# Kernel optimization log

Measured on AMD Instinct MI355X. Metric: run time of the kernel, lower is better.

The kernel has to match this reference:

```python
import jax, jax.numpy as jnp
import numpy as np

B, N, L, E = 4, 8, 2048, 16384
CH = [128, 256, 256, 256]
EPS = 1e-5
USE_MAX = True


def setup_inputs() -> dict:
    key = jax.random.key(0)
    ks = jax.random.split(key, 10)
    d = {}
    d["x"] = jax.random.normal(ks[0], (B, N, CH[0], L), jnp.float32)
    d["edge_index"] = jax.random.randint(ks[1], (2, E), 0, L, dtype=jnp.int32)
    wspecs = [("W1", CH[0], CH[1]), ("W2", CH[1], CH[2]), ("W3", CH[2], CH[3]),
              ("W1s", CH[0], CH[1]), ("W2s", CH[1], CH[2]), ("W3s", CH[2], CH[3])]
    for i, (nm, ci, co) in enumerate(wspecs):
        std = (2.0 / (ci + co)) ** 0.5  # xavier_normal
        d[nm] = std * jax.random.normal(ks[2 + i], (ci, co), jnp.float32)
        d["b" + nm[1:]] = jnp.zeros((co,), jnp.float32)
    for nm, co in [("1", CH[1]), ("2", CH[2]), ("3", CH[3]),
                   ("1s", CH[1]), ("2s", CH[2]), ("3s", CH[3])]:
        d["g" + nm] = jnp.ones((co,), jnp.float32)
        d["be" + nm] = jnp.zeros((co,), jnp.float32)
    return d


def _gcn_norm(edge_index, num_nodes):
    # PyG gcn_norm with improved=True: A_hat = A + 2I, sym normalization.
    src, dst = edge_index[0], edge_index[1]
    loop = jnp.arange(num_nodes, dtype=src.dtype)
    src = jnp.concatenate([src, loop])
    dst = jnp.concatenate([dst, loop])
    w = jnp.concatenate([jnp.ones((edge_index.shape[1],), jnp.float32),
                         jnp.full((num_nodes,), 2.0, jnp.float32)])
    deg = jnp.zeros((num_nodes,), jnp.float32).at[dst].add(w)
    dis = jnp.where(deg > 0, jax.lax.rsqrt(deg), 0.0)
    return src, dst, dis[src] * w * dis[dst]


def _gcn(h, W, bias, src, dst, norm, num_nodes):
    # h: [G, L, Cin] node features for G independent copies of the shared graph
    hw = h @ W  # [G, L, Cout]
    msgs = hw[:, src, :] * norm[None, :, None]  # gather along nodes
    agg = jnp.zeros((h.shape[0], num_nodes, W.shape[1]), h.dtype).at[:, dst].add(msgs)
    return agg + bias


def _bn(x, g, be):
    # x: [Nb, C, L]; training-mode BatchNorm1d over (Nb, L) per channel
    m = x.mean(axis=(0, 2), keepdims=True)
    v = x.var(axis=(0, 2), keepdims=True)
    return g[None, :, None] * (x - m) * jax.lax.rsqrt(v + EPS) + be[None, :, None]


def _forward(x, edge_index, params):
    b, n, c, l = x.shape
    src, dst, norm = _gcn_norm(edge_index, l)
    xo = None
    for (W, bias, Ws, bs, g, be, gs, bes) in params:
        # per-element branch
        h = x.reshape(b * n, x.shape[2], l).transpose(0, 2, 1)  # [b*n, L, C]
        x1 = _gcn(h, W, bias, src, dst, norm, l).transpose(0, 2, 1)  # [b*n, Cout, L]
        x1 = _bn(x1, g, be)
        # symmetric pooled branch
        xp = jnp.max(x, axis=1) if USE_MAX else jnp.sum(x, axis=1)  # [b, C, L]
        x2 = _gcn(xp.transpose(0, 2, 1), Ws, bs, src, dst, norm, l).transpose(0, 2, 1)
        x2 = _bn(x2, gs, bes)
        co = x2.shape[1]
        x2 = jnp.broadcast_to(x2[:, None], (b, n, co, l)).reshape(b * n, co, l)
        xo = jax.nn.relu(x1 + x2)  # [b*n, Cout, L]
        x = xo.reshape(b, n, co, l)
    return xo  # final output is [b*n, CH[3], L] (not reshaped back)


def reference(x, edge_index, W1, b1, W2, b2, W3, b3, W1s, b1s, W2s, b2s, W3s, b3s,
              g1, be1, g2, be2, g3, be3, g1s, be1s, g2s, be2s, g3s, be3s):
    params = [(W1, b1, W1s, b1s, g1, be1, g1s, be1s),
              (W2, b2, W2s, b2s, g2, be2, g2s, be2s),
              (W3, b3, W3s, b3s, g3, be3, g3s, be3s)]
    return _forward(x, edge_index, params)
```

## Files before the change

kernel.cpp:

```cpp
#include <hip/hip_runtime.h>
#include <math.h>

#define LNODES 2048
#define NEDGE 16384
#define GBIG 32
#define GSM 4
#define NCOUT 256
#define BN_EPS 1e-5f
#define ND 32

typedef unsigned short u16;
typedef __attribute__((ext_vector_type(8))) short bf16x8;
typedef __attribute__((ext_vector_type(4))) float f32x4;

__device__ __forceinline__ unsigned pk2(float a, float b) {
  unsigned ua = __float_as_uint(a); ua += 0x7fffu + ((ua >> 16) & 1u);
  unsigned ub = __float_as_uint(b); ub += 0x7fffu + ((ub >> 16) & 1u);
  return (ua >> 16) | (ub & 0xffff0000u);
}
__device__ __forceinline__ float blo(unsigned u) { return __uint_as_float(u << 16); }
__device__ __forceinline__ float bhi(unsigned u) { return __uint_as_float(u & 0xffff0000u); }


__global__ __launch_bounds__(256) void count_deg_k(const int* __restrict__ ei,
                                                   float* __restrict__ deg,
                                                   int* __restrict__ cnt) {
  int e = blockIdx.x * 256 + threadIdx.x;
  if (e < NEDGE) {
    int d = ei[NEDGE + e];
    atomicAdd(&deg[d], 1.0f);
    atomicAdd(&cnt[d], 1);
  }
}

__global__ __launch_bounds__(256) void dis_k(const float* __restrict__ deg,
                                             float* __restrict__ dis,
                                             float* __restrict__ selfn) {
  int i = blockIdx.x * 256 + threadIdx.x;
  if (i < LNODES) {
    float di = rsqrtf(deg[i] + 2.0f);
    dis[i] = di;
    selfn[i] = 2.0f * di * di;
  }
}

__global__ __launch_bounds__(256) void scan_k(const int* __restrict__ cnt,
                                              int* __restrict__ rp) {
  __shared__ int part[256];
  int t = threadIdx.x;
  int base = t * 8;
  int loc[8];
  int s = 0;
#pragma unroll
  for (int j = 0; j < 8; ++j) { loc[j] = s; s += cnt[base + j]; }
  part[t] = s;
  __syncthreads();
  for (int off = 1; off < 256; off <<= 1) {
    int v = (t >= off) ? part[t - off] : 0;
    __syncthreads();
    part[t] += v;
    __syncthreads();
  }
  int excl = (t == 0) ? 0 : part[t - 1];
#pragma unroll
  for (int j = 0; j < 8; ++j) rp[base + j] = excl + loc[j];
  if (t == 255) rp[LNODES] = part[255];
}

__global__ __launch_bounds__(256) void fill_k(const int* __restrict__ ei,
                                              const int* __restrict__ rp,
                                              int* __restrict__ fillc,
                                              const float* __restrict__ dis,
                                              int* __restrict__ col,
                                              float* __restrict__ wn) {
  int e = blockIdx.x * 256 + threadIdx.x;
  if (e < NEDGE) {
    int s = ei[e], d = ei[NEDGE + e];
    int pos = rp[d] + atomicAdd(&fillc[d], 1);
    col[pos] = s;
    wn[pos] = dis[s] * dis[d];
  }
}

__global__ __launch_bounds__(256) void trans_k(const float* __restrict__ X,
                                               u16* __restrict__ XT, int Cin) {
  __shared__ float T[64][65];
  const int g = blockIdx.z;
  const int n0 = blockIdx.x * 64;
  const int c0 = blockIdx.y * 64;
  const int tr = threadIdx.x >> 4;
  const int tc = (threadIdx.x & 15) * 4;
#pragma unroll
  for (int p = 0; p < 4; ++p) {
    int ci = c0 + tr + p * 16;
    float4 v = *reinterpret_cast<const float4*>(&X[((size_t)g * Cin + ci) * LNODES + n0 + tc]);
    T[tr + p * 16][tc + 0] = v.x; T[tr + p * 16][tc + 1] = v.y;
    T[tr + p * 16][tc + 2] = v.z; T[tr + p * 16][tc + 3] = v.w;
  }
  __syncthreads();
#pragma unroll
  for (int p = 0; p < 4; ++p) {
    int nd = tr + p * 16;
    uint2 o = {pk2(T[tc + 0][nd], T[tc + 1][nd]), pk2(T[tc + 2][nd], T[tc + 3][nd])};
    *reinterpret_cast<uint2*>(&XT[((size_t)g * LNODES + n0 + nd) * Cin + c0 + tc]) = o;
  }
}

struct WCvt {
  const float* src[6];
  u16* dst[6];
  int ci[6];
};
__global__ __launch_bounds__(256) void cvtw_all_k(WCvt wp) {
  __shared__ float T[64][65];
  const int w = blockIdx.z;
  const int Ci = wp.ci[w];
  const int ci0 = blockIdx.y * 64;
  if (ci0 >= Ci) return;
  const float* W = wp.src[w];
  u16* WT = wp.dst[w];
  const int co0 = blockIdx.x * 64;
  const int tr = threadIdx.x >> 4;
  const int tc = (threadIdx.x & 15) * 4;
#pragma unroll
  for (int p = 0; p < 4; ++p) {
    int ci = ci0 + tr + p * 16;
    float4 v = *reinterpret_cast<const float4*>(&W[(size_t)ci * NCOUT + co0 + tc]);
    T[tr + p * 16][tc + 0] = v.x; T[tr + p * 16][tc + 1] = v.y;
    T[tr + p * 16][tc + 2] = v.z; T[tr + p * 16][tc + 3] = v.w;
  }
  __syncthreads();
#pragma unroll
  for (int p = 0; p < 4; ++p) {
    int co = tr + p * 16;
    uint2 o = {pk2(T[tc + 0][co], T[tc + 1][co]), pk2(T[tc + 2][co], T[tc + 3][co])};
    *reinterpret_cast<uint2*>(&WT[(size_t)(co0 + co) * Ci + ci0 + tc]) = o;
  }
}

__global__ __launch_bounds__(256) void pool_bf_k(const u16* __restrict__ X,
                                                 u16* __restrict__ XP, int per) {
  int i = blockIdx.x * 256 + threadIdx.x;
  size_t f = (size_t)i * 8;
  int b = (int)(f / per);
  size_t rem = f - (size_t)b * per;
  const u16* base = X + (size_t)b * 8 * per + rem;
  uint4 u = *reinterpret_cast<const uint4*>(base);
  float m0 = blo(u.x), m1 = bhi(u.x), m2 = blo(u.y), m3 = bhi(u.y);
  float m4 = blo(u.z), m5 = bhi(u.z), m6 = blo(u.w), m7 = bhi(u.w);
#pragma unroll
  for (int j = 1; j < 8; ++j) {
    uint4 v = *reinterpret_cast<const uint4*>(base + (size_t)j * per);
    m0 = fmaxf(m0, blo(v.x)); m1 = fmaxf(m1, bhi(v.x));
    m2 = fmaxf(m2, blo(v.y)); m3 = fmaxf(m3, bhi(v.y));
    m4 = fmaxf(m4, blo(v.z)); m5 = fmaxf(m5, bhi(v.z));
    m6 = fmaxf(m6, blo(v.w)); m7 = fmaxf(m7, bhi(v.w));
  }
  uint4 o = {pk2(m0, m1), pk2(m2, m3), pk2(m4, m5), pk2(m6, m7)};
  *reinterpret_cast<uint4*>(XP + (size_t)b * per + rem) = o;
}

__device__ __forceinline__ void coef_ld(const float* __restrict__ st,
                                        const float* __restrict__ ga,
                                        const float* __restrict__ be,
                                        const float* __restrict__ gs,
                                        const float* __restrict__ bes,
                                        float* lk1, float* lk2, float* lcc, int t) {
  float sA = 0.f, qA = 0.f, sB = 0.f, qB = 0.f;
#pragma unroll
  for (int x = 0; x < 8; ++x) {
    sA += st[x * NCOUT + t];
    qA += st[2048 + x * NCOUT + t];
    sB += st[4096 + x * NCOUT + t];
    qB += st[6144 + x * NCOUT + t];
  }
  const float c1 = (float)(GBIG * LNODES), c2 = (float)(GSM * LNODES);
  float mA = sA / c1;
  float vA = qA / c1 - mA * mA;
  float kA = ga[t] * rsqrtf(vA + BN_EPS);
  float mB = sB / c2;
  float vB = qB / c2 - mB * mB;
  float kB = gs[t] * rsqrtf(vB + BN_EPS);
  lk1[t] = kA;
  lk2[t] = kB;
  lcc[t] = be[t] - kA * mA + bes[t] - kB * mB;
}

template <int MODE>
__global__ __launch_bounds__(256) void gemm2_k(const u16* __restrict__ B1,
                                               const u16* __restrict__ B2,
                                               const float* __restrict__ st,
                                               const float* __restrict__ ga,
                                               const float* __restrict__ be,
                                               const float* __restrict__ gs,
                                               const float* __restrict__ bes,
                                               const u16* __restrict__ WbT,
                                               const u16* __restrict__ WsT,
                                               u16* __restrict__ HW1,
                                               u16* __restrict__ hw2) {
  constexpr int Cin = (MODE == 0) ? 128 : 256;
  constexpr int BT = 64 * Cin;
  constexpr int EPI = 64 * 264;
  constexpr int SMSZ = (BT > EPI) ? BT : EPI;
  __shared__ u16 smem[SMSZ];
  __shared__ float lk1[NCOUT], lk2[NCOUT], lcc[NCOUT];
  const int z = blockIdx.z;
  const bool sym = z < GSM;
  const int g = sym ? z : z - GSM;
  const u16* Wmat = sym ? WsT : WbT;
  u16* out = sym ? hw2 : HW1;
  const int n0 = blockIdx.x * 64;
  const int t = threadIdx.x;
  constexpr int OPR = Cin / 8;
  constexpr int RPI = 256 / OPR;
  constexpr int NIT = 64 / RPI;
  const int ro = t / OPR;
  const int ch8 = (t % OPR) * 8;

  float K1[8], K2[8], CC[8];
  if constexpr (MODE == 1) {
    coef_ld(st, ga, be, gs, bes, lk1, lk2, lcc, t);
    __syncthreads();
#pragma unroll
    for (int j = 0; j < 8; ++j) { K1[j] = lk1[ch8 + j]; K2[j] = lk2[ch8 + j]; CC[j] = lcc[ch8 + j]; }
  }

#define BIDX(r, c) ((((r) * Cin) + (c)) ^ (((r) & 7) << 3))

  if constexpr (MODE == 0) {
    const u16* src = (sym ? B2 : B1) + (size_t)g * LNODES * Cin;
#pragma unroll
    for (int it = 0; it < NIT; ++it) {
      int row = it * RPI + ro;
      uint4 v = *reinterpret_cast<const uint4*>(&src[(size_t)(n0 + row) * Cin + ch8]);
      *reinterpret_cast<uint4*>(&smem[BIDX(row, ch8)]) = v;
    }
  } else if (!sym) {
    const size_t b1o = ((size_t)g * LNODES + n0) * NCOUT + ch8;
    const size_t b2o = ((size_t)(g >> 3) * LNODES + n0) * NCOUT + ch8;
#pragma unroll
    for (int it = 0; it < NIT; ++it) {
      int row = it * RPI + ro;
      uint4 a1 = *reinterpret_cast<const uint4*>(&B1[b1o + (size_t)row * NCOUT]);
      uint4 a2 = *reinterpret_cast<const uint4*>(&B2[b2o + (size_t)row * NCOUT]);
      float o0 = fmaxf(K1[0] * blo(a1.x) + K2[0] * blo(a2.x) + CC[0], 0.f);
      float o1 = fmaxf(K1[1] * bhi(a1.x) + K2[1] * bhi(a2.x) + CC[1], 0.f);
      float o2 = fmaxf(K1[2] * blo(a1.y) + K2[2] * blo(a2.y) + CC[2], 0.f);
      float o3 = fmaxf(K1[3] * bhi(a1.y) + K2[3] * bhi(a2.y) + CC[3], 0.f);
      float o4 = fmaxf(K1[4] * blo(a1.z) + K2[4] * blo(a2.z) + CC[4], 0.f);
      float o5 = fmaxf(K1[5] * bhi(a1.z) + K2[5] * bhi(a2.z) + CC[5], 0.f);
      float o6 = fmaxf(K1[6] * blo(a1.w) + K2[6] * blo(a2.w) + CC[6], 0.f);
      float o7 = fmaxf(K1[7] * bhi(a1.w) + K2[7] * bhi(a2.w) + CC[7], 0.f);
      uint4 ov = {pk2(o0, o1), pk2(o2, o3), pk2(o4, o5), pk2(o6, o7)};
      *reinterpret_cast<uint4*>(&smem[BIDX(row, ch8)]) = ov;
    }
  } else {
    const size_t b2o = ((size_t)g * LNODES + n0) * NCOUT + ch8;
    const size_t a1b = ((size_t)(g * 8) * LNODES + n0) * NCOUT + ch8;
    const size_t nstep = (size_t)LNODES * NCOUT;
    for (int it = 0; it < NIT; ++it) {
      int row = it * RPI + ro;
      uint4 a2 = *reinterpret_cast<const uint4*>(&B2[b2o + (size_t)row * NCOUT]);
      float t0 = K2[0] * blo(a2.x) + CC[0], t1 = K2[1] * bhi(a2.x) + CC[1];
      float t2 = K2[2] * blo(a2.y) + CC[2], t3 = K2[3] * bhi(a2.y) + CC[3];
      float t4 = K2[4] * blo(a2.z) + CC[4], t5 = K2[5] * bhi(a2.z) + CC[5];
      float t6 = K2[6] * blo(a2.w) + CC[6], t7 = K2[7] * bhi(a2.w) + CC[7];
      float m0 = 0.f, m1 = 0.f, m2 = 0.f, m3 = 0.f, m4 = 0.f, m5 = 0.f, m6 = 0.f, m7 = 0.f;
#pragma unroll
      for (int n = 0; n < 8; ++n) {
        uint4 a1 = *reinterpret_cast<const uint4*>(&B1[a1b + n * nstep + (size_t)row * NCOUT]);
        m0 = fmaxf(m0, K1[0] * blo(a1.x) + t0); m1 = fmaxf(m1, K1[1] * bhi(a1.x) + t1);
        m2 = fmaxf(m2, K1[2] * blo(a1.y) + t2); m3 = fmaxf(m3, K1[3] * bhi(a1.y) + t3);
        m4 = fmaxf(m4, K1[4] * blo(a1.z) + t4); m5 = fmaxf(m5, K1[5] * bhi(a1.z) + t5);
        m6 = fmaxf(m6, K1[6] * blo(a1.w) + t6); m7 = fmaxf(m7, K1[7] * bhi(a1.w) + t7);
      }
      uint4 ov = {pk2(m0, m1), pk2(m2, m3), pk2(m4, m5), pk2(m6, m7)};
      *reinterpret_cast<uint4*>(&smem[BIDX(row, ch8)]) = ov;
    }
  }
  __syncthreads();

  const int wv = t >> 6;
  const int lane = t & 63;
  const int q = lane >> 4, l = lane & 15;
  f32x4 zero = {0.f, 0.f, 0.f, 0.f};
  f32x4 acc[4][4];
#pragma unroll
  for (int i = 0; i < 4; ++i)
#pragma unroll
    for (int j = 0; j < 4; ++j) acc[i][j] = zero;

  const u16* Wfrag = Wmat + (size_t)(wv * 64 + l) * Cin + q * 8;
#pragma unroll
  for (int k0 = 0; k0 < Cin; k0 += 32) {
    bf16x8 af[4], bx[4];
#pragma unroll
    for (int fi = 0; fi < 4; ++fi)
      af[fi] = *reinterpret_cast<const bf16x8*>(&Wfrag[(size_t)(fi * 16) * Cin + k0]);
#pragma unroll
    for (int fj = 0; fj < 4; ++fj) {
      int brow = fj * 16 + l;
      bx[fj] = *reinterpret_cast<const bf16x8*>(&smem[(brow * Cin + k0 + q * 8) ^ ((brow & 7) << 3)]);
    }
#pragma unroll
    for (int fi = 0; fi < 4; ++fi)
#pragma unroll
      for (int fj = 0; fj < 4; ++fj)
        acc[fi][fj] = __builtin_amdgcn_mfma_f32_16x16x32_bf16(af[fi], bx[fj], acc[fi][fj], 0, 0, 0);
  }
#undef BIDX

  __syncthreads();
  u16* Csh = smem;
#pragma unroll
  for (int fi = 0; fi < 4; ++fi) {
#pragma unroll
    for (int fj = 0; fj < 4; ++fj) {
      int co_l = wv * 64 + fi * 16 + q * 4;
      int nd_l = fj * 16 + l;
      uint2 pkd = {pk2(acc[fi][fj][0], acc[fi][fj][1]),
                   pk2(acc[fi][fj][2], acc[fi][fj][3])};
      *reinterpret_cast<uint2*>(&Csh[nd_l * 264 + co_l]) = pkd;
    }
  }
  __syncthreads();
#pragma unroll
  for (int p = 0; p < 8; ++p) {
    int idx = p * 256 + t;
    int nd = idx >> 5;
    int c8 = (idx & 31) * 8;
    uint4 v = *reinterpret_cast<const uint4*>(&Csh[nd * 264 + c8]);
    *reinterpret_cast<uint4*>(&out[((size_t)g * LNODES + n0 + nd) * NCOUT + c8]) = v;
  }
}

__global__ __launch_bounds__(256) void agg_comb_k(const u16* __restrict__ HW1,
                                                  const u16* __restrict__ hw2,
                                                  const int* __restrict__ col,
                                                  const float* __restrict__ wn,
                                                  const int* __restrict__ rp,
                                                  const float* __restrict__ selfn,
                                                  u16* __restrict__ AGG1,
                                                  u16* __restrict__ agg2,
                                                  float* __restrict__ st) {
  __shared__ float lsum[8][NCOUT], lsq[8][NCOUT];
  const int bid = blockIdx.x;
  const int t = threadIdx.x;
  const int wv = t >> 6;
  float* sumO;
  float* sqO;
  int shard;
  if (bid < 1024) {
    int slot = bid >> 3;
    int chunk = slot & 63;
    int g0 = (bid & 7) + 8 * (slot >> 6);
    const int d0 = chunk * ND;
    const int h = (t >> 5) & 1;
    const int ch = (t & 31) * 8;
    const u16* baseh = HW1 + (size_t)(g0 + 16 * h) * LNODES * NCOUT;
    u16* outh = AGG1 + (size_t)(g0 + 16 * h) * LNODES * NCOUT;
    float s0 = 0.f, s1 = 0.f, s2 = 0.f, s3 = 0.f, s4 = 0.f, s5 = 0.f, s6 = 0.f, s7 = 0.f;
    float q0 = 0.f, q1 = 0.f, q2 = 0.f, q3 = 0.f, q4 = 0.f, q5 = 0.f, q6 = 0.f, q7 = 0.f;
    for (int i = wv; i < ND; i += 4) {
      int d = d0 + i;
      int e0 = rp[d], e1 = rp[d + 1];
      float sw = selfn[d];
      uint4 u = *reinterpret_cast<const uint4*>(&baseh[(size_t)d * NCOUT + ch]);
      float a0 = sw * blo(u.x), a1 = sw * bhi(u.x), a2 = sw * blo(u.y), a3 = sw * bhi(u.y);
      float a4 = sw * blo(u.z), a5 = sw * bhi(u.z), a6 = sw * blo(u.w), a7 = sw * bhi(u.w);
      int e = e0;
      const int e4 = e0 + ((e1 - e0) & ~3);
      for (; e < e4; e += 4) {
        int i0 = col[e + 0], i1 = col[e + 1], i2 = col[e + 2], i3 = col[e + 3];
        float w0 = wn[e + 0], w1 = wn[e + 1], w2 = wn[e + 2], w3 = wn[e + 3];
        uint4 v0 = *reinterpret_cast<const uint4*>(&baseh[(size_t)i0 * NCOUT + ch]);
        uint4 v1 = *reinterpret_cast<const uint4*>(&baseh[(size_t)i1 * NCOUT + ch]);
        uint4 v2 = *reinterpret_cast<const uint4*>(&baseh[(size_t)i2 * NCOUT + ch]);
        uint4 v3 = *reinterpret_cast<const uint4*>(&baseh[(size_t)i3 * NCOUT + ch]);
        a0 += w0 * blo(v0.x); a1 += w0 * bhi(v0.x); a2 += w0 * blo(v0.y); a3 += w0 * bhi(v0.y);
        a4 += w0 * blo(v0.z); a5 += w0 * bhi(v0.z); a6 += w0 * blo(v0.w); a7 += w0 * bhi(v0.w);
        a0 += w1 * blo(v1.x); a1 += w1 * bhi(v1.x); a2 += w1 * blo(v1.y); a3 += w1 * bhi(v1.y);
        a4 += w1 * blo(v1.z); a5 += w1 * bhi(v1.z); a6 += w1 * blo(v1.w); a7 += w1 * bhi(v1.w);
        a0 += w2 * blo(v2.x); a1 += w2 * bhi(v2.x); a2 += w2 * blo(v2.y); a3 += w2 * bhi(v2.y);
        a4 += w2 * blo(v2.z); a5 += w2 * bhi(v2.z); a6 += w2 * blo(v2.w); a7 += w2 * bhi(v2.w);
        a0 += w3 * blo(v3.x); a1 += w3 * bhi(v3.x); a2 += w3 * blo(v3.y); a3 += w3 * bhi(v3.y);
        a4 += w3 * blo(v3.z); a5 += w3 * bhi(v3.z); a6 += w3 * blo(v3.w); a7 += w3 * bhi(v3.w);
      }
      for (; e < e1; ++e) {
        int ci = col[e];
        float w = wn[e];
        uint4 v = *reinterpret_cast<const uint4*>(&baseh[(size_t)ci * NCOUT + ch]);
        a0 += w * blo(v.x); a1 += w * bhi(v.x); a2 += w * blo(v.y); a3 += w * bhi(v.y);
        a4 += w * blo(v.z); a5 += w * bhi(v.z); a6 += w * blo(v.w); a7 += w * bhi(v.w);
      }
      uint4 o = {pk2(a0, a1), pk2(a2, a3), pk2(a4, a5), pk2(a6, a7)};
      *reinterpret_cast<uint4*>(&outh[(size_t)d * NCOUT + ch]) = o;
      s0 += a0; s1 += a1; s2 += a2; s3 += a3; s4 += a4; s5 += a5; s6 += a6; s7 += a7;
      q0 += a0 * a0; q1 += a1 * a1; q2 += a2 * a2; q3 += a3 * a3;
      q4 += a4 * a4; q5 += a5 * a5; q6 += a6 * a6; q7 += a7 * a7;
    }
    int row = wv * 2 + h;
    float4 sa = {s0, s1, s2, s3}, sb = {s4, s5, s6, s7};
    float4 qa = {q0, q1, q2, q3}, qb = {q4, q5, q6, q7};
    *reinterpret_cast<float4*>(&lsum[row][ch]) = sa;
    *reinterpret_cast<float4*>(&lsum[row][ch + 4]) = sb;
    *reinterpret_cast<float4*>(&lsq[row][ch]) = qa;
    *reinterpret_cast<float4*>(&lsq[row][ch + 4]) = qb;
    sumO = st; sqO = st + 2048; shard = (bid & 7) * NCOUT;
  } else {
    int b2 = bid - 1024;
    int g = b2 & (GSM - 1);
    int chunk = b2 >> 2;
    const int d0 = chunk * ND;
    const int lc = (t & 63) * 4;
    const u16* base = hw2 + (size_t)g * LNODES * NCOUT;
    float4 s = {0.f, 0.f, 0.f, 0.f}, qq = {0.f, 0.f, 0.f, 0.f};
    for (int i = wv; i < ND; i += 4) {
      int d = d0 + i;
      int e0 = rp[d], e1 = rp[d + 1];
      float sw = selfn[d];
      uint2 u = *reinterpret_cast<const uint2*>(&base[(size_t)d * NCOUT + lc]);
      float4 a = {sw * blo(u.x), sw * bhi(u.x), sw * blo(u.y), sw * bhi(u.y)};
      int e = e0;
      const int e4 = e0 + ((e1 - e0) & ~3);
      for (; e < e4; e += 4) {
        int i0 = col[e + 0], i1 = col[e + 1], i2 = col[e + 2], i3 = col[e + 3];
        float w0 = wn[e + 0], w1 = wn[e + 1], w2 = wn[e + 2], w3 = wn[e + 3];
        uint2 v0 = *reinterpret_cast<const uint2*>(&base[(size_t)i0 * NCOUT + lc]);
        uint2 v1 = *reinterpret_cast<const uint2*>(&base[(size_t)i1 * NCOUT + lc]);
        uint2 v2 = *reinterpret_cast<const uint2*>(&base[(size_t)i2 * NCOUT + lc]);
        uint2 v3 = *reinterpret_cast<const uint2*>(&base[(size_t)i3 * NCOUT + lc]);
        a.x += w0 * blo(v0.x); a.y += w0 * bhi(v0.x); a.z += w0 * blo(v0.y); a.w += w0 * bhi(v0.y);
        a.x += w1 * blo(v1.x); a.y += w1 * bhi(v1.x); a.z += w1 * blo(v1.y); a.w += w1 * bhi(v1.y);
        a.x += w2 * blo(v2.x); a.y += w2 * bhi(v2.x); a.z += w2 * blo(v2.y); a.w += w2 * bhi(v2.y);
        a.x += w3 * blo(v3.x); a.y += w3 * bhi(v3.x); a.z += w3 * blo(v3.y); a.w += w3 * bhi(v3.y);
      }
      for (; e < e1; ++e) {
        float w = wn[e];
        uint2 v = *reinterpret_cast<const uint2*>(&base[(size_t)col[e] * NCOUT + lc]);
        a.x += w * blo(v.x); a.y += w * bhi(v.x); a.z += w * blo(v.y); a.w += w * bhi(v.y);
      }
      uint2 o = {pk2(a.x, a.y), pk2(a.z, a.w)};
      *reinterpret_cast<uint2*>(&agg2[((size_t)g * LNODES + d) * NCOUT + lc]) = o;
      s.x += a.x; s.y += a.y; s.z += a.z; s.w += a.w;
      qq.x += a.x * a.x; qq.y += a.y * a.y; qq.z += a.z * a.z; qq.w += a.w * a.w;
    }
    *reinterpret_cast<float4*>(&lsum[wv][lc]) = s;
    *reinterpret_cast<float4*>(&lsq[wv][lc]) = qq;
    float4 z4 = {0.f, 0.f, 0.f, 0.f};
    *reinterpret_cast<float4*>(&lsum[wv + 4][lc]) = z4;
    *reinterpret_cast<float4*>(&lsq[wv + 4][lc]) = z4;
    sumO = st + 4096; sqO = st + 6144; shard = (b2 & 7) * NCOUT;
  }
  __syncthreads();
  float ts = 0.f, tq = 0.f;
#pragma unroll
  for (int r = 0; r < 8; ++r) {
    ts += lsum[r][t];
    tq += lsq[r][t];
  }
  atomicAdd(&sumO[shard + t], ts);
  atomicAdd(&sqO[shard + t], tq);
}

__global__ __launch_bounds__(256) void fuse_tr_bf_k(const u16* __restrict__ A1,
                                                    const u16* __restrict__ A2,
                                                    const float* __restrict__ st,
                                                    const float* __restrict__ ga,
                                                    const float* __restrict__ be,
                                                    const float* __restrict__ gs,
                                                    const float* __restrict__ bes,
                                                    float* __restrict__ O) {
  __shared__ float T[64][65];
  __shared__ float lk1[NCOUT], lk2[NCOUT], lcc[NCOUT];
  const int g = blockIdx.z;
  const int d0 = blockIdx.x * 64;
  const int c0 = blockIdx.y * 64;
  const int b = g >> 3;
  const int t = threadIdx.x;
  coef_ld(st, ga, be, gs, bes, lk1, lk2, lcc, t);
  __syncthreads();
  const int tr = t >> 4;
  const int tc = (t & 15) * 4;
#pragma unroll
  for (int p = 0; p < 4; ++p) {
    int d = d0 + tr + p * 16;
    uint2 a1 = *reinterpret_cast<const uint2*>(&A1[((size_t)g * LNODES + d) * NCOUT + c0 + tc]);
    uint2 a2 = *reinterpret_cast<const uint2*>(&A2[((size_t)b * LNODES + d) * NCOUT + c0 + tc]);
    int cb = c0 + tc;
    T[tr + p * 16][tc + 0] = fmaxf(lk1[cb+0] * blo(a1.x) + lk2[cb+0] * blo(a2.x) + lcc[cb+0], 0.f);
    T[tr + p * 16][tc + 1] = fmaxf(lk1[cb+1] * bhi(a1.x) + lk2[cb+1] * bhi(a2.x) + lcc[cb+1], 0.f);
    T[tr + p * 16][tc + 2] = fmaxf(lk1[cb+2] * blo(a1.y) + lk2[cb+2] * blo(a2.y) + lcc[cb+2], 0.f);
    T[tr + p * 16][tc + 3] = fmaxf(lk1[cb+3] * bhi(a1.y) + lk2[cb+3] * bhi(a2.y) + lcc[cb+3], 0.f);
  }
  __syncthreads();
#pragma unroll
  for (int p = 0; p < 4; ++p) {
    int c = tr + p * 16;
    float4 o = {T[tc + 0][c], T[tc + 1][c], T[tc + 2][c], T[tc + 3][c]};
    *reinterpret_cast<float4*>(&O[((size_t)g * NCOUT + c0 + c) * LNODES + d0 + tc]) = o;
  }
}


extern "C" void kernel_launch(void* const* d_in, const int* in_sizes, int n_in,
                              void* d_out, int out_size, void* d_ws, size_t ws_size,
                              hipStream_t stream) {
  const float* x_in = (const float*)d_in[0];
  const int* ei = (const int*)d_in[1];
  const float* W[3]   = {(const float*)d_in[2],  (const float*)d_in[4],  (const float*)d_in[6]};
  const float* Wsym[3]= {(const float*)d_in[8],  (const float*)d_in[10], (const float*)d_in[12]};
  const float* ga[3]  = {(const float*)d_in[14], (const float*)d_in[16], (const float*)d_in[18]};
  const float* be[3]  = {(const float*)d_in[15], (const float*)d_in[17], (const float*)d_in[19]};
  const float* gs[3]  = {(const float*)d_in[20], (const float*)d_in[22], (const float*)d_in[24]};
  const float* bes[3] = {(const float*)d_in[21], (const float*)d_in[23], (const float*)d_in[25]};

  const size_t EBIG = (size_t)GBIG * LNODES * NCOUT;
  const size_t ESM = (size_t)GSM * LNODES * NCOUT;
  char* p = (char*)d_ws;
  u16* XT0  = (u16*)p; p += (size_t)GBIG * LNODES * 128 * 2;
  u16* AGG1 = (u16*)p; p += EBIG * 2;
  u16* agg2 = (u16*)p; p += ESM * 2;
  u16* xp   = (u16*)p; p += ESM * 2;
  u16* hw2  = (u16*)p; p += ESM * 2;
  u16* WbT[3], *WsT[3];
  for (int i = 0; i < 3; ++i) { WbT[i] = (u16*)p; p += NCOUT * NCOUT * 2; }
  for (int i = 0; i < 3; ++i) { WsT[i] = (u16*)p; p += NCOUT * NCOUT * 2; }
  int*   rp   = (int*)p;   p += 2064 * 4;
  float* dis  = (float*)p; p += LNODES * 4;
  float* selfn= (float*)p; p += LNODES * 4;
  char* zbase = p;
  float* deg  = (float*)p; p += LNODES * 4;
  int*   cnt  = (int*)p;   p += LNODES * 4;
  int*   fillc= (int*)p;   p += LNODES * 4;
  int*   col  = (int*)p;   p += (NEDGE + 8) * 4;
  float* wn   = (float*)p; p += (NEDGE + 8) * 4;
  float* stats= (float*)p; p += 3 * 4 * 2048 * 4;
  size_t zsize = (size_t)(p - zbase);

  u16* HW1 = (u16*)d_out;
  float* stL[3] = {stats, stats + 8192, stats + 16384};

  hipMemsetAsync(zbase, 0, zsize, stream);
  count_deg_k<<<NEDGE / 256, 256, 0, stream>>>(ei, deg, cnt);
  dis_k<<<LNODES / 256, 256, 0, stream>>>(deg, dis, selfn);
  scan_k<<<1, 256, 0, stream>>>(cnt, rp);
  fill_k<<<NEDGE / 256, 256, 0, stream>>>(ei, rp, fillc, dis, col, wn);
  WCvt wc;
  for (int i = 0; i < 3; ++i) {
    wc.src[i] = W[i];     wc.dst[i] = WbT[i];     wc.ci[i] = (i == 0) ? 128 : 256;
    wc.src[3 + i] = Wsym[i]; wc.dst[3 + i] = WsT[i]; wc.ci[3 + i] = (i == 0) ? 128 : 256;
  }
  cvtw_all_k<<<dim3(4, 4, 6), 256, 0, stream>>>(wc);
  trans_k<<<dim3(LNODES / 64, 128 / 64, GBIG), 256, 0, stream>>>(x_in, XT0, 128);
  pool_bf_k<<<GSM * 128 * LNODES / 8 / 256, 256, 0, stream>>>(XT0, xp, 128 * LNODES);

  dim3 ggrid(LNODES / 64, 1, GBIG + GSM);
  gemm2_k<0><<<ggrid, 256, 0, stream>>>(XT0, xp, nullptr, nullptr, nullptr, nullptr,
                                        nullptr, WbT[0], WsT[0], HW1, hw2);
  agg_comb_k<<<1280, 256, 0, stream>>>(HW1, hw2, col, wn, rp, selfn, AGG1, agg2, stL[0]);
  gemm2_k<1><<<ggrid, 256, 0, stream>>>(AGG1, agg2, stL[0], ga[0], be[0], gs[0], bes[0],
                                        WbT[1], WsT[1], HW1, hw2);
  agg_comb_k<<<1280, 256, 0, stream>>>(HW1, hw2, col, wn, rp, selfn, AGG1, agg2, stL[1]);
  gemm2_k<1><<<ggrid, 256, 0, stream>>>(AGG1, agg2, stL[1], ga[1], be[1], gs[1], bes[1],
                                        WbT[2], WsT[2], HW1, hw2);
  agg_comb_k<<<1280, 256, 0, stream>>>(HW1, hw2, col, wn, rp, selfn, AGG1, agg2, stL[2]);
  fuse_tr_bf_k<<<dim3(LNODES / 64, NCOUT / 64, GBIG), 256, 0, stream>>>(
      AGG1, agg2, stL[2], ga[2], be[2], gs[2], bes[2], (float*)d_out);
}
```

Before: 357.7 us.

## Stage weight K-tiles into LDS via direct global-to-LDS loads in GEMM

Weights are pre-converted into a K-tiled, XOR-swizzled layout with 32-wide K slices. The GEMM stages each 256x32 slice into shared memory with global_load_lds, then reads A fragments from LDS instead of issuing strided global loads per wave. The goal is to cut uncoalesced global weight traffic and latency in the MFMA loop. The cost is two barriers per K step and 16 KB of extra LDS per block, which may lower occupancy and serialise loading with compute.

```diff
diff --git a/kernel.cpp b/kernel.cpp
--- a/kernel.cpp
+++ b/kernel.cpp
@@ -20,6 +20,12 @@
 }
 __device__ __forceinline__ float blo(unsigned u) { return __uint_as_float(u << 16); }
 __device__ __forceinline__ float bhi(unsigned u) { return __uint_as_float(u & 0xffff0000u); }
+
+__device__ __forceinline__ void gl16(const u16* g, u16* l) {
+  __builtin_amdgcn_global_load_lds(
+      (const __attribute__((address_space(1))) void*)g,
+      (__attribute__((address_space(3))) void*)l, 16, 0, 0);
+}
 
 
 __global__ __launch_bounds__(256) void count_deg_k(const int* __restrict__ ei,
@@ -130,11 +136,16 @@
     T[tr + p * 16][tc + 2] = v.z; T[tr + p * 16][tc + 3] = v.w;
   }
   __syncthreads();
+  const int ci = ci0 + tc;
+  const int kt = ci >> 5;
+  const int kk = ci & 31;
 #pragma unroll
   for (int p = 0; p < 4; ++p) {
-    int co = tr + p * 16;
-    uint2 o = {pk2(T[tc + 0][co], T[tc + 1][co]), pk2(T[tc + 2][co], T[tc + 3][co])};
-    *reinterpret_cast<uint2*>(&WT[(size_t)(co0 + co) * Ci + ci0 + tc]) = o;
+    int co = co0 + tr + p * 16;
+    uint2 o = {pk2(T[tc + 0][co - co0], T[tc + 1][co - co0]),
+               pk2(T[tc + 2][co - co0], T[tc + 3][co - co0])};
+    size_t idx = (size_t)kt * 8192 + (unsigned)((co * 32 + kk) ^ ((co & 7) << 3));
+    *reinterpret_cast<uint2*>(&WT[idx]) = o;
   }
 }
 
@@ -187,7 +198,7 @@
 }
 
 template <int MODE>
-__global__ __launch_bounds__(256) void gemm2_k(const u16* __restrict__ B1,
+__global__ __launch_bounds__(256) void gemm3_k(const u16* __restrict__ B1,
                                                const u16* __restrict__ B2,
                                                const float* __restrict__ st,
                                                const float* __restrict__ ga,
@@ -199,15 +210,15 @@
                                                u16* __restrict__ HW1,
                                                u16* __restrict__ hw2) {
   constexpr int Cin = (MODE == 0) ? 128 : 256;
-  constexpr int BT = 64 * Cin;
+  constexpr int BSH = 64 * Cin;
   constexpr int EPI = 64 * 264;
-  constexpr int SMSZ = (BT > EPI) ? BT : EPI;
-  __shared__ u16 smem[SMSZ];
+  constexpr int BASE = (BSH > EPI) ? BSH : EPI;
+  __shared__ __align__(16) u16 smem[BASE + 8192];
   __shared__ float lk1[NCOUT], lk2[NCOUT], lcc[NCOUT];
+  u16* Wsh = smem + BASE;
   const int z = blockIdx.z;
   const bool sym = z < GSM;
   const int g = sym ? z : z - GSM;
-  const u16* Wmat = sym ? WsT : WbT;
   u16* out = sym ? hw2 : HW1;
   const int n0 = blockIdx.x * 64;
   const int t = threadIdx.x;
@@ -227,15 +238,40 @@
 
 #define BIDX(r, c) ((((r) * Cin) + (c)) ^ (((r) & 7) << 3))
 
-  if constexpr (MODE == 0) {
-    const u16* src = (sym ? B2 : B1) + (size_t)g * LNODES * Cin;
-#pragma unroll
-    for (int it = 0; it < NIT; ++it) {
-      int row = it * RPI + ro;
-      uint4 v = *reinterpret_cast<const uint4*>(&src[(size_t)(n0 + row) * Cin + ch8]);
-      *reinterpret_cast<uint4*>(&smem[BIDX(row, ch8)]) = v;
-    }
-  } else if (!sym) {
+  if (MODE == 0 || sym) {
+    if constexpr (MODE == 0) {
+      const u16* src = (sym ? B2 : B1) + ((size_t)g * LNODES + n0) * Cin + ch8;
+#pragma unroll
+      for (int it = 0; it < NIT; ++it) {
+        int row = it * RPI + ro;
+        uint4 v = *reinterpret_cast<const uint4*>(&src[(size_t)row * Cin]);
+        *reinterpret_cast<uint4*>(&smem[BIDX(row, ch8)]) = v;
+      }
+    } else {
+      const size_t b2o = ((size_t)g * LNODES + n0) * NCOUT + ch8;
+      const size_t a1b = ((size_t)(g * 8) * LNODES + n0) * NCOUT + ch8;
+      const size_t nstep = (size_t)LNODES * NCOUT;
+      for (int it = 0; it < NIT; ++it) {
+        int row = it * RPI + ro;
+        uint4 a2 = *reinterpret_cast<const uint4*>(&B2[b2o + (size_t)row * NCOUT]);
+        float t0 = K2[0] * blo(a2.x) + CC[0], t1 = K2[1] * bhi(a2.x) + CC[1];
+        float t2 = K2[2] * blo(a2.y) + CC[2], t3 = K2[3] * bhi(a2.y) + CC[3];
+        float t4 = K2[4] * blo(a2.z) + CC[4], t5 = K2[5] * bhi(a2.z) + CC[5];
+        float t6 = K2[6] * blo(a2.w) + CC[6], t7 = K2[7] * bhi(a2.w) + CC[7];
+        float m0 = 0.f, m1 = 0.f, m2 = 0.f, m3 = 0.f, m4 = 0.f, m5 = 0.f, m6 = 0.f, m7 = 0.f;
+#pragma unroll
+        for (int n = 0; n < 8; ++n) {
+          uint4 a1 = *reinterpret_cast<const uint4*>(&B1[a1b + n * nstep + (size_t)row * NCOUT]);
+          m0 = fmaxf(m0, K1[0] * blo(a1.x) + t0); m1 = fmaxf(m1, K1[1] * bhi(a1.x) + t1);
+          m2 = fmaxf(m2, K1[2] * blo(a1.y) + t2); m3 = fmaxf(m3, K1[3] * bhi(a1.y) + t3);
+          m4 = fmaxf(m4, K1[4] * blo(a1.z) + t4); m5 = fmaxf(m5, K1[5] * bhi(a1.z) + t5);
+          m6 = fmaxf(m6, K1[6] * blo(a1.w) + t6); m7 = fmaxf(m7, K1[7] * bhi(a1.w) + t7);
+        }
+        uint4 ov = {pk2(m0, m1), pk2(m2, m3), pk2(m4, m5), pk2(m6, m7)};
+        *reinterpret_cast<uint4*>(&smem[BIDX(row, ch8)]) = ov;
+      }
+    }
+  } else {
     const size_t b1o = ((size_t)g * LNODES + n0) * NCOUT + ch8;
     const size_t b2o = ((size_t)(g >> 3) * LNODES + n0) * NCOUT + ch8;
 #pragma unroll
@@ -254,31 +290,7 @@
       uint4 ov = {pk2(o0, o1), pk2(o2, o3), pk2(o4, o5), pk2(o6, o7)};
       *reinterpret_cast<uint4*>(&smem[BIDX(row, ch8)]) = ov;
     }
-  } else {
-    const size_t b2o = ((size_t)g * LNODES + n0) * NCOUT + ch8;
-    const size_t a1b = ((size_t)(g * 8) * LNODES + n0) * NCOUT + ch8;
-    const size_t nstep = (size_t)LNODES * NCOUT;
-    for (int it = 0; it < NIT; ++it) {
-      int row = it * RPI + ro;
-      uint4 a2 = *reinterpret_cast<const uint4*>(&B2[b2o + (size_t)row * NCOUT]);
-      float t0 = K2[0] * blo(a2.x) + CC[0], t1 = K2[1] * bhi(a2.x) + CC[1];
-      float t2 = K2[2] * blo(a2.y) + CC[2], t3 = K2[3] * bhi(a2.y) + CC[3];
-      float t4 = K2[4] * blo(a2.z) + CC[4], t5 = K2[5] * bhi(a2.z) + CC[5];
-      float t6 = K2[6] * blo(a2.w) + CC[6], t7 = K2[7] * bhi(a2.w) + CC[7];
-      float m0 = 0.f, m1 = 0.f, m2 = 0.f, m3 = 0.f, m4 = 0.f, m5 = 0.f, m6 = 0.f, m7 = 0.f;
-#pragma unroll
-      for (int n = 0; n < 8; ++n) {
-        uint4 a1 = *reinterpret_cast<const uint4*>(&B1[a1b + n * nstep + (size_t)row * NCOUT]);
-        m0 = fmaxf(m0, K1[0] * blo(a1.x) + t0); m1 = fmaxf(m1, K1[1] * bhi(a1.x) + t1);
-        m2 = fmaxf(m2, K1[2] * blo(a1.y) + t2); m3 = fmaxf(m3, K1[3] * bhi(a1.y) + t3);
-        m4 = fmaxf(m4, K1[4] * blo(a1.z) + t4); m5 = fmaxf(m5, K1[5] * bhi(a1.z) + t5);
-        m6 = fmaxf(m6, K1[6] * blo(a1.w) + t6); m7 = fmaxf(m7, K1[7] * bhi(a1.w) + t7);
-      }
-      uint4 ov = {pk2(m0, m1), pk2(m2, m3), pk2(m4, m5), pk2(m6, m7)};
-      *reinterpret_cast<uint4*>(&smem[BIDX(row, ch8)]) = ov;
-    }
-  }
-  __syncthreads();
+  }
 
   const int wv = t >> 6;
   const int lane = t & 63;
@@ -290,17 +302,25 @@
 #pragma unroll
     for (int j = 0; j < 4; ++j) acc[i][j] = zero;
 
-  const u16* Wfrag = Wmat + (size_t)(wv * 64 + l) * Cin + q * 8;
-#pragma unroll
-  for (int k0 = 0; k0 < Cin; k0 += 32) {
+  const u16* Wmat = sym ? WsT : WbT;
+#pragma unroll
+  for (int kt = 0; kt < Cin / 32; ++kt) {
+    __syncthreads();
+    const u16* ws = Wmat + (size_t)kt * 8192;
+#pragma unroll
+    for (int c = 0; c < 4; ++c)
+      gl16(ws + c * 2048 + t * 8, &Wsh[c * 2048 + t * 8]);
+    __syncthreads();
     bf16x8 af[4], bx[4];
 #pragma unroll
-    for (int fi = 0; fi < 4; ++fi)
-      af[fi] = *reinterpret_cast<const bf16x8*>(&Wfrag[(size_t)(fi * 16) * Cin + k0]);
+    for (int fi = 0; fi < 4; ++fi) {
+      int row = wv * 64 + fi * 16 + l;
+      af[fi] = *reinterpret_cast<const bf16x8*>(&Wsh[(row * 32 + q * 8) ^ ((row & 7) << 3)]);
+    }
 #pragma unroll
     for (int fj = 0; fj < 4; ++fj) {
       int brow = fj * 16 + l;
-      bx[fj] = *reinterpret_cast<const bf16x8*>(&smem[(brow * Cin + k0 + q * 8) ^ ((brow & 7) << 3)]);
+      bx[fj] = *reinterpret_cast<const bf16x8*>(&smem[BIDX(brow, kt * 32 + q * 8)]);
     }
 #pragma unroll
     for (int fi = 0; fi < 4; ++fi)
@@ -556,13 +576,13 @@
   pool_bf_k<<<GSM * 128 * LNODES / 8 / 256, 256, 0, stream>>>(XT0, xp, 128 * LNODES);
 
   dim3 ggrid(LNODES / 64, 1, GBIG + GSM);
-  gemm2_k<0><<<ggrid, 256, 0, stream>>>(XT0, xp, nullptr, nullptr, nullptr, nullptr,
+  gemm3_k<0><<<ggrid, 256, 0, stream>>>(XT0, xp, nullptr, nullptr, nullptr, nullptr,
                                         nullptr, WbT[0], WsT[0], HW1, hw2);
   agg_comb_k<<<1280, 256, 0, stream>>>(HW1, hw2, col, wn, rp, selfn, AGG1, agg2, stL[0]);
-  gemm2_k<1><<<ggrid, 256, 0, stream>>>(AGG1, agg2, stL[0], ga[0], be[0], gs[0], bes[0],
+  gemm3_k<1><<<ggrid, 256, 0, stream>>>(AGG1, agg2, stL[0], ga[0], be[0], gs[0], bes[0],
                                         WbT[1], WsT[1], HW1, hw2);
   agg_comb_k<<<1280, 256, 0, stream>>>(HW1, hw2, col, wn, rp, selfn, AGG1, agg2, stL[1]);
-  gemm2_k<1><<<ggrid, 256, 0, stream>>>(AGG1, agg2, stL[1], ga[1], be[1], gs[1], bes[1],
+  gemm3_k<1><<<ggrid, 256, 0, stream>>>(AGG1, agg2, stL[1], ga[1], be[1], gs[1], bes[1],
                                         WbT[2], WsT[2], HW1, hw2);
   agg_comb_k<<<1280, 256, 0, stream>>>(HW1, hw2, col, wn, rp, selfn, AGG1, agg2, stL[2]);
   fuse_tr_bf_k<<<dim3(LNODES / 64, NCOUT / 64, GBIG), 256, 0, stream>>>(
```

After: 344.9 us. 1.04x faster.
